# Optimization experiments

Hardware: AMD Instinct MI355X
Metric: run time of the kernel (lower is better)

Reference implementation:

```python
import jax, jax.numpy as jnp
import numpy as np

B, T, D = 32, 4096, 512  # batch, encoder timesteps t_k, attn_sz (== encoder dim == state_sz)


def setup_inputs() -> dict:
    key = jax.random.key(0)
    ks = jax.random.split(key, 7)
    scale = 1.0 / np.sqrt(D)
    return {
        "h_i": jax.random.normal(ks[0], (B, T, D), dtype=jnp.float32),
        "s_t": jax.random.normal(ks[1], (B, D), dtype=jnp.float32),
        "coverage": jax.random.uniform(ks[2], (B, T), dtype=jnp.float32),
        "W_h": jax.random.normal(ks[3], (D, D), dtype=jnp.float32) * scale,
        "W_s": jax.random.normal(ks[4], (D, D), dtype=jnp.float32) * scale,
        "b_s": jnp.zeros((D,), dtype=jnp.float32),
        "W_c": jax.random.normal(ks[5], (1, D), dtype=jnp.float32) * scale,
        "V": jax.random.normal(ks[6], (D, 1), dtype=jnp.float32) * scale,
    }


def reference(h_i, s_t, coverage, W_h, W_s, b_s, W_c, V):
    # enc_features: (B, T, D)
    enc_features = jnp.einsum("btd,de->bte", h_i, W_h)
    # dec_features: (B, D) broadcast over T
    dec_features = s_t @ W_s + b_s
    # coverage term: Dense(D) applied to coverage[..., None] -> outer product with W_c row
    cov_features = coverage[..., None] * W_c[0]  # (B, T, D)
    features = enc_features + dec_features[:, None, :] + cov_features
    # e_t = V(tanh(features)) squeezed to (B, T)
    e_t = jnp.einsum("bte,e->bt", jnp.tanh(features), V[:, 0])
    a_t = jax.nn.softmax(e_t, axis=1)  # (B, T)
    new_coverage = coverage + a_t
    # context = a_t^T h_i : (B, D)
    context_vector = jnp.einsum("bt,btd->bd", a_t, h_i)
    return context_vector, a_t, new_coverage
```

## Files before the change

kernel.cpp:

```cpp
#include <hip/hip_runtime.h>
#include <stdint.h>

#define B_ 32
#define T_ 4096
#define D_ 512
#define BT_ (B_*T_)

typedef __attribute__((ext_vector_type(8))) short bf16x8;
typedef __attribute__((ext_vector_type(4))) float f32x4;

__device__ __forceinline__ unsigned short f2bf(float f) {
    unsigned int u = __float_as_uint(f);
    u += 0x7FFFu + ((u >> 16) & 1u);
    return (unsigned short)(u >> 16);
}

__device__ __forceinline__ float tanh_fast(float x) {
    float e2 = __expf(2.0f * x);
    return 1.0f - 2.0f / (e2 + 1.0f);
}

__global__ __launch_bounds__(256) void k_conv_wh(const float* __restrict__ W_h,
                                                 unsigned short* __restrict__ wsb) {
    int tid = blockIdx.x * 256 + threadIdx.x;
    int l  = tid & 63;
    int kt = (tid >> 6) & 15;
    int nt = tid >> 10;
    int n  = nt * 16 + (l & 15);
    int k0 = kt * 32 + (l >> 4) * 8;
    unsigned int w[4];
#pragma unroll
    for (int q = 0; q < 4; ++q) {
        unsigned short lo = f2bf(W_h[(size_t)(k0 + 2*q)     * D_ + n]);
        unsigned short hi = f2bf(W_h[(size_t)(k0 + 2*q + 1) * D_ + n]);
        w[q] = (unsigned int)lo | ((unsigned int)hi << 16);
    }
    uint4 pk = {w[0], w[1], w[2], w[3]};
    ((uint4*)wsb)[tid] = pk;
}

__global__ __launch_bounds__(256) void k_dec(const float* __restrict__ s_t,
                                             const float* __restrict__ W_s,
                                             const float* __restrict__ b_s,
                                             float* __restrict__ dec) {
    int b = blockIdx.x;
    int c = threadIdx.x;
    float a0 = b_s[c], a1 = b_s[c + 256];
    const float* srow = s_t + b * D_;
    for (int k = 0; k < D_; ++k) {
        float s = srow[k];
        const float* wr = W_s + (size_t)k * D_;
        a0 = fmaf(s, wr[c], a0);
        a1 = fmaf(s, wr[c + 256], a1);
    }
    dec[b * D_ + c] = a0;
    dec[b * D_ + c + 256] = a1;
}

__global__ __launch_bounds__(512, 4) void k_main(const float* __restrict__ h_i,
                                                 const float* __restrict__ coverage,
                                                 const unsigned short* __restrict__ wsb,
                                                 const float* __restrict__ dec,
                                                 const float* __restrict__ W_c,
                                                 const float* __restrict__ V,
                                                 float* __restrict__ e_out) {
    __shared__ __align__(16) unsigned char As[65536];
    __shared__ float red[8][64];
    const int tid = threadIdx.x;
    const int w = tid >> 6, l = tid & 63;
    const int row0 = blockIdx.x * 64;
    const int b    = row0 >> 12;
    const int t0   = row0 & (T_ - 1);

#pragma unroll
    for (int i = 0; i < 8; ++i) {
        int row = i * 8 + w;
        const float* src = h_i + (size_t)(row0 + row) * D_ + l * 8;
        float4 f0 = *(const float4*)(src);
        float4 f1 = *(const float4*)(src + 4);
        uint4 pk;
        pk.x = (unsigned)f2bf(f0.x) | ((unsigned)f2bf(f0.y) << 16);
        pk.y = (unsigned)f2bf(f0.z) | ((unsigned)f2bf(f0.w) << 16);
        pk.z = (unsigned)f2bf(f1.x) | ((unsigned)f2bf(f1.y) << 16);
        pk.w = (unsigned)f2bf(f1.z) | ((unsigned)f2bf(f1.w) << 16);
        int kt   = l >> 2;
        int lam  = (row & 15) + 16 * (l & 3);
        int slot = (lam & 0x38) | ((lam & 7) ^ ((l & 3) << 1) ^ (kt & 1));
        int byte = (((row >> 4) * 16 + kt) << 10) + (slot << 4);
        *(uint4*)(As + byte) = pk;
    }
    __syncthreads();

    const int slotR = (l & 0x38) | ((l & 7) ^ (((l >> 4) & 3) << 1));

    f32x4 acc[4][4];
#pragma unroll
    for (int af = 0; af < 4; ++af)
#pragma unroll
        for (int j = 0; j < 4; ++j) acc[af][j] = (f32x4){0, 0, 0, 0};

    const uint4* bw = (const uint4*)wsb + ((w * 4) << 10) + l;

#pragma unroll 4
    for (int kt = 0; kt < 16; ++kt) {
        bf16x8 bv[4];
#pragma unroll
        for (int j = 0; j < 4; ++j) {
            uint4 braw = bw[(j << 10) + (kt << 6)];
            bv[j] = __builtin_bit_cast(bf16x8, braw);
        }
        int sl = (slotR ^ (kt & 1)) << 4;
#pragma unroll
        for (int af = 0; af < 4; ++af) {
            int byte = ((af * 16 + kt) << 10) + sl;
            uint4 araw = *(const uint4*)(As + byte);
            bf16x8 a = __builtin_bit_cast(bf16x8, araw);
#pragma unroll
            for (int j = 0; j < 4; ++j)
                acc[af][j] = __builtin_amdgcn_mfma_f32_16x16x32_bf16(a, bv[j], acc[af][j], 0, 0, 0);
        }
    }

    const int rgrp = (l >> 4) * 4;
    float cov_r[4][4];
#pragma unroll
    for (int af = 0; af < 4; ++af)
#pragma unroll
        for (int r = 0; r < 4; ++r)
            cov_r[af][r] = coverage[b * T_ + t0 + af * 16 + rgrp + r];

    float p[4][4] = {{0,0,0,0},{0,0,0,0},{0,0,0,0},{0,0,0,0}};
#pragma unroll
    for (int j = 0; j < 4; ++j) {
        int col = w * 64 + j * 16 + (l & 15);
        float dv = dec[b * D_ + col];
        float wc = W_c[col];
        float vv = V[col];
#pragma unroll
        for (int af = 0; af < 4; ++af)
#pragma unroll
            for (int r = 0; r < 4; ++r) {
                float x = acc[af][j][r] + dv + cov_r[af][r] * wc;
                p[af][r] += tanh_fast(x) * vv;
            }
    }

#pragma unroll
    for (int m = 1; m <= 8; m <<= 1)
#pragma unroll
        for (int af = 0; af < 4; ++af)
#pragma unroll
            for (int r = 0; r < 4; ++r)
                p[af][r] += __shfl_xor(p[af][r], m, 64);
    if ((l & 15) == 0) {
#pragma unroll
        for (int af = 0; af < 4; ++af)
#pragma unroll
            for (int r = 0; r < 4; ++r)
                red[w][af * 16 + rgrp + r] = p[af][r];
    }
    __syncthreads();
    if (tid < 64) {
        float e = red[0][tid] + red[1][tid] + red[2][tid] + red[3][tid]
                + red[4][tid] + red[5][tid] + red[6][tid] + red[7][tid];
        e_out[b * T_ + t0 + tid] = e;
    }
}

__global__ __launch_bounds__(256) void k_soft(const float* __restrict__ e_in,
                                              const float* __restrict__ coverage,
                                              float* __restrict__ out_at,
                                              float* __restrict__ out_cov) {
    int b = blockIdx.x, tid = threadIdx.x;
    __shared__ float red[4];
    float v[16];
    float m = -1e30f;
#pragma unroll
    for (int i = 0; i < 16; ++i) {
        v[i] = e_in[b * T_ + tid + i * 256];
        m = fmaxf(m, v[i]);
    }
#pragma unroll
    for (int mk = 1; mk <= 32; mk <<= 1) m = fmaxf(m, __shfl_xor(m, mk, 64));
    if ((tid & 63) == 0) red[tid >> 6] = m;
    __syncthreads();
    m = fmaxf(fmaxf(red[0], red[1]), fmaxf(red[2], red[3]));
    float s = 0.f;
#pragma unroll
    for (int i = 0; i < 16; ++i) { v[i] = expf(v[i] - m); s += v[i]; }
#pragma unroll
    for (int mk = 1; mk <= 32; mk <<= 1) s += __shfl_xor(s, mk, 64);
    __syncthreads();
    if ((tid & 63) == 0) red[tid >> 6] = s;
    __syncthreads();
    s = red[0] + red[1] + red[2] + red[3];
    float inv = 1.0f / s;
#pragma unroll
    for (int i = 0; i < 16; ++i) {
        int idx = b * T_ + tid + i * 256;
        float a = v[i] * inv;
        out_at[idx]  = a;
        out_cov[idx] = coverage[idx] + a;
    }
}

__global__ __launch_bounds__(256) void k_ctx(const float* __restrict__ h_i,
                                             const float* __restrict__ a_t,
                                             float* __restrict__ part) {
    int blk = blockIdx.x;
    int b = blk >> 6, s = blk & 63;
    int d0 = threadIdx.x * 2;
    const size_t base = ((size_t)b * T_ + (size_t)s * 64) * D_;
    const float* at = a_t + b * T_ + s * 64;
    float2 acc = {0.f, 0.f};
    for (int t = 0; t < 64; ++t) {
        float a = at[t];
        float2 h2 = *(const float2*)(h_i + base + (size_t)t * D_ + d0);
        acc.x = fmaf(a, h2.x, acc.x);
        acc.y = fmaf(a, h2.y, acc.y);
    }
    float* pp = part + (size_t)blk * D_ + d0;
    pp[0] = acc.x;
    pp[1] = acc.y;
}

__global__ __launch_bounds__(256) void k_comb(const float* __restrict__ part,
                                              float* __restrict__ out_ctx) {
    int idx = blockIdx.x * 256 + threadIdx.x;
    int b = idx >> 9, d = idx & 511;
    const float* pp = part + (size_t)b * 64 * D_ + d;
    float s = 0.f;
#pragma unroll 8
    for (int j = 0; j < 64; ++j) s += pp[(size_t)j * D_];
    out_ctx[idx] = s;
}

extern "C" void kernel_launch(void* const* d_in, const int* in_sizes, int n_in,
                              void* d_out, int out_size, void* d_ws, size_t ws_size,
                              hipStream_t stream) {
    const float* h_i      = (const float*)d_in[0];
    const float* s_t      = (const float*)d_in[1];
    const float* coverage = (const float*)d_in[2];
    const float* W_h      = (const float*)d_in[3];
    const float* W_s      = (const float*)d_in[4];
    const float* b_s      = (const float*)d_in[5];
    const float* W_c      = (const float*)d_in[6];
    const float* V        = (const float*)d_in[7];

    float* out_ctx = (float*)d_out;
    float* out_at  = out_ctx + B_ * D_;
    float* out_cov = out_at + BT_;

    unsigned short* wsb = (unsigned short*)d_ws;
    float* dec  = (float*)((char*)d_ws + 524288);
    float* part = dec + B_ * D_;

    k_conv_wh<<<128, 256, 0, stream>>>(W_h, wsb);
    k_dec<<<B_, 256, 0, stream>>>(s_t, W_s, b_s, dec);
    k_main<<<BT_ / 64, 512, 0, stream>>>(h_i, coverage, wsb, dec, W_c, V, out_at);
    k_soft<<<B_, 256, 0, stream>>>(out_at, coverage, out_at, out_cov);
    k_ctx<<<B_ * 64, 256, 0, stream>>>(h_i, out_at, part);
    k_comb<<<B_ * D_ / 256, 256, 0, stream>>>(part, out_ctx);
}
```

Measured before the change: 196.1 us.

## Split A-tile staging into two K halves and overlap second load with MFMA

```diff
diff --git a/kernel.cpp b/kernel.cpp
--- a/kernel.cpp
+++ b/kernel.cpp
@@ -72,54 +72,88 @@
     const int b    = row0 >> 12;
     const int t0   = row0 & (T_ - 1);
 
+    const int s_ktl  = l >> 3;
+    const int s_m    = ((l >> 1) & 3);
+    const int s_bits = (s_m << 4) | (w ^ (s_m << 1) ^ (l >> 3 & 1));
+    const int s_off  = (s_ktl << 10) + ((l & 1) << 3);
+
+    const int slotR = (l & 0x38) | ((l & 7) ^ (((l >> 4) & 3) << 1));
+
+    const uint4* bw = (const uint4*)wsb + ((w * 4) << 10) + l;
+
+    f32x4 acc[4][4];
+#pragma unroll
+    for (int af = 0; af < 4; ++af)
+#pragma unroll
+        for (int j = 0; j < 4; ++j) acc[af][j] = (f32x4){0, 0, 0, 0};
+
+    float4 L[8];
+#pragma unroll
+    for (int i = 0; i < 8; ++i)
+        L[i] = *(const float4*)(h_i + (size_t)(row0 + i * 8 + w) * D_ + l * 4);
+
+    unsigned char* A0 = As;
+    unsigned char* A1 = As + 32768;
 #pragma unroll
     for (int i = 0; i < 8; ++i) {
-        int row = i * 8 + w;
-        const float* src = h_i + (size_t)(row0 + row) * D_ + l * 8;
-        float4 f0 = *(const float4*)(src);
-        float4 f1 = *(const float4*)(src + 4);
-        uint4 pk;
-        pk.x = (unsigned)f2bf(f0.x) | ((unsigned)f2bf(f0.y) << 16);
-        pk.y = (unsigned)f2bf(f0.z) | ((unsigned)f2bf(f0.w) << 16);
-        pk.z = (unsigned)f2bf(f1.x) | ((unsigned)f2bf(f1.y) << 16);
-        pk.w = (unsigned)f2bf(f1.z) | ((unsigned)f2bf(f1.w) << 16);
-        int kt   = l >> 2;
-        int lam  = (row & 15) + 16 * (l & 3);
-        int slot = (lam & 0x38) | ((lam & 7) ^ ((l & 3) << 1) ^ (kt & 1));
-        int byte = (((row >> 4) * 16 + kt) << 10) + (slot << 4);
-        *(uint4*)(As + byte) = pk;
-    }
-    __syncthreads();
-
-    const int slotR = (l & 0x38) | ((l & 7) ^ (((l >> 4) & 3) << 1));
-
-    f32x4 acc[4][4];
-#pragma unroll
-    for (int af = 0; af < 4; ++af)
-#pragma unroll
-        for (int j = 0; j < 4; ++j) acc[af][j] = (f32x4){0, 0, 0, 0};
-
-    const uint4* bw = (const uint4*)wsb + ((w * 4) << 10) + l;
-
-#pragma unroll 4
-    for (int kt = 0; kt < 16; ++kt) {
-        bf16x8 bv[4];
-#pragma unroll
-        for (int j = 0; j < 4; ++j) {
-            uint4 braw = bw[(j << 10) + (kt << 6)];
-            bv[j] = __builtin_bit_cast(bf16x8, braw);
+        uint2 pk;
+        pk.x = (unsigned)f2bf(L[i].x) | ((unsigned)f2bf(L[i].y) << 16);
+        pk.y = (unsigned)f2bf(L[i].z) | ((unsigned)f2bf(L[i].w) << 16);
+        int slot = ((i & 1) << 3) | s_bits;
+        int byte = (((i >> 1) << 13)) + (slot << 4) + s_off;
+        *(uint2*)(A0 + byte) = pk;
+    }
+
+    float4 M[8];
+#pragma unroll
+    for (int i = 0; i < 8; ++i)
+        M[i] = *(const float4*)(h_i + (size_t)(row0 + i * 8 + w) * D_ + 256 + l * 4);
+
+    asm volatile("s_waitcnt lgkmcnt(0)" ::: "memory");
+    __builtin_amdgcn_s_barrier();
+
+    auto compute = [&](const unsigned char* Ab, int h8) {
+        uint4 bp[2][4];
+#pragma unroll
+        for (int j = 0; j < 4; ++j) bp[0][j] = bw[(j << 10) + ((h8 + 0) << 6)];
+#pragma unroll
+        for (int j = 0; j < 4; ++j) bp[1][j] = bw[(j << 10) + ((h8 + 1) << 6)];
+#pragma unroll
+        for (int ktl = 0; ktl < 8; ++ktl) {
+            const int sl = ((slotR ^ (ktl & 1)) << 4);
+#pragma unroll
+            for (int af = 0; af < 4; ++af) {
+                uint4 araw = *(const uint4*)(Ab + ((af * 8 + ktl) << 10) + sl);
+                bf16x8 a = __builtin_bit_cast(bf16x8, araw);
+#pragma unroll
+                for (int j = 0; j < 4; ++j) {
+                    bf16x8 bv = __builtin_bit_cast(bf16x8, bp[ktl & 1][j]);
+                    acc[af][j] = __builtin_amdgcn_mfma_f32_16x16x32_bf16(a, bv, acc[af][j], 0, 0, 0);
+                }
+            }
+            if (ktl < 6) {
+#pragma unroll
+                for (int j = 0; j < 4; ++j)
+                    bp[ktl & 1][j] = bw[(j << 10) + ((h8 + ktl + 2) << 6)];
+            }
         }
-        int sl = (slotR ^ (kt & 1)) << 4;
-#pragma unroll
-        for (int af = 0; af < 4; ++af) {
-            int byte = ((af * 16 + kt) << 10) + sl;
-            uint4 araw = *(const uint4*)(As + byte);
-            bf16x8 a = __builtin_bit_cast(bf16x8, araw);
-#pragma unroll
-            for (int j = 0; j < 4; ++j)
-                acc[af][j] = __builtin_amdgcn_mfma_f32_16x16x32_bf16(a, bv[j], acc[af][j], 0, 0, 0);
-        }
-    }
+    };
+
+    compute(A0, 0);
+
+#pragma unroll
+    for (int i = 0; i < 8; ++i) {
+        uint2 pk;
+        pk.x = (unsigned)f2bf(M[i].x) | ((unsigned)f2bf(M[i].y) << 16);
+        pk.y = (unsigned)f2bf(M[i].z) | ((unsigned)f2bf(M[i].w) << 16);
+        int slot = ((i & 1) << 3) | s_bits;
+        int byte = (((i >> 1) << 13)) + (slot << 4) + s_off;
+        *(uint2*)(A1 + byte) = pk;
+    }
+    asm volatile("s_waitcnt lgkmcnt(0)" ::: "memory");
+    __builtin_amdgcn_s_barrier();
+
+    compute(A1, 8);
 
     const int rgrp = (l >> 4) * 4;
     float cov_r[4][4];
```

After: 241.7 us. +23.3%, slower.

## Fuse context accumulation into attention-score kernel using unnormalized exp weights

Applied to the files above, without the earlier changes.

```diff
diff --git a/kernel.cpp b/kernel.cpp
--- a/kernel.cpp
+++ b/kernel.cpp
@@ -63,31 +63,41 @@
                                                  const float* __restrict__ dec,
                                                  const float* __restrict__ W_c,
                                                  const float* __restrict__ V,
-                                                 float* __restrict__ e_out) {
+                                                 float* __restrict__ e_out,
+                                                 float* __restrict__ part) {
     __shared__ __align__(16) unsigned char As[65536];
     __shared__ float red[8][64];
+    __shared__ float wexp[64];
     const int tid = threadIdx.x;
     const int w = tid >> 6, l = tid & 63;
     const int row0 = blockIdx.x * 64;
     const int b    = row0 >> 12;
     const int t0   = row0 & (T_ - 1);
 
+    float4 L0[8], L1[8];
 #pragma unroll
     for (int i = 0; i < 8; ++i) {
-        int row = i * 8 + w;
-        const float* src = h_i + (size_t)(row0 + row) * D_ + l * 8;
-        float4 f0 = *(const float4*)(src);
-        float4 f1 = *(const float4*)(src + 4);
-        uint4 pk;
-        pk.x = (unsigned)f2bf(f0.x) | ((unsigned)f2bf(f0.y) << 16);
-        pk.y = (unsigned)f2bf(f0.z) | ((unsigned)f2bf(f0.w) << 16);
-        pk.z = (unsigned)f2bf(f1.x) | ((unsigned)f2bf(f1.y) << 16);
-        pk.w = (unsigned)f2bf(f1.z) | ((unsigned)f2bf(f1.w) << 16);
-        int kt   = l >> 2;
-        int lam  = (row & 15) + 16 * (l & 3);
-        int slot = (lam & 0x38) | ((lam & 7) ^ ((l & 3) << 1) ^ (kt & 1));
-        int byte = (((row >> 4) * 16 + kt) << 10) + (slot << 4);
-        *(uint4*)(As + byte) = pk;
+        const float* src = h_i + (size_t)(row0 + i * 8 + w) * D_ + l * 8;
+        L0[i] = *(const float4*)(src);
+        L1[i] = *(const float4*)(src + 4);
+    }
+    {
+        const int kt   = l >> 2;
+        const int lam  = 16 * (l & 3);
+        const int sl_m = (l & 3) << 1;
+#pragma unroll
+        for (int i = 0; i < 8; ++i) {
+            int row = i * 8 + w;
+            uint4 pk;
+            pk.x = (unsigned)f2bf(L0[i].x) | ((unsigned)f2bf(L0[i].y) << 16);
+            pk.y = (unsigned)f2bf(L0[i].z) | ((unsigned)f2bf(L0[i].w) << 16);
+            pk.z = (unsigned)f2bf(L1[i].x) | ((unsigned)f2bf(L1[i].y) << 16);
+            pk.w = (unsigned)f2bf(L1[i].z) | ((unsigned)f2bf(L1[i].w) << 16);
+            int lamf = lam + (row & 15);
+            int slot = (lamf & 0x38) | ((lamf & 7) ^ sl_m ^ (kt & 1));
+            int byte = (((row >> 4) * 16 + kt) << 10) + (slot << 4);
+            *(uint4*)(As + byte) = pk;
+        }
     }
     __syncthreads();
 
@@ -101,23 +111,30 @@
 
     const uint4* bw = (const uint4*)wsb + ((w * 4) << 10) + l;
 
-#pragma unroll 4
-    for (int kt = 0; kt < 16; ++kt) {
-        bf16x8 bv[4];
-#pragma unroll
-        for (int j = 0; j < 4; ++j) {
-            uint4 braw = bw[(j << 10) + (kt << 6)];
-            bv[j] = __builtin_bit_cast(bf16x8, braw);
-        }
-        int sl = (slotR ^ (kt & 1)) << 4;
-#pragma unroll
-        for (int af = 0; af < 4; ++af) {
-            int byte = ((af * 16 + kt) << 10) + sl;
-            uint4 araw = *(const uint4*)(As + byte);
-            bf16x8 a = __builtin_bit_cast(bf16x8, araw);
-#pragma unroll
-            for (int j = 0; j < 4; ++j)
-                acc[af][j] = __builtin_amdgcn_mfma_f32_16x16x32_bf16(a, bv[j], acc[af][j], 0, 0, 0);
+    {
+        uint4 bp[2][4];
+#pragma unroll
+        for (int j = 0; j < 4; ++j) bp[0][j] = bw[(j << 10)];
+#pragma unroll
+        for (int j = 0; j < 4; ++j) bp[1][j] = bw[(j << 10) + (1 << 6)];
+#pragma unroll
+        for (int kt = 0; kt < 16; ++kt) {
+            const int sl = ((slotR ^ (kt & 1)) << 4);
+#pragma unroll
+            for (int af = 0; af < 4; ++af) {
+                uint4 araw = *(const uint4*)(As + ((af * 16 + kt) << 10) + sl);
+                bf16x8 a = __builtin_bit_cast(bf16x8, araw);
+#pragma unroll
+                for (int j = 0; j < 4; ++j) {
+                    bf16x8 bv = __builtin_bit_cast(bf16x8, bp[kt & 1][j]);
+                    acc[af][j] = __builtin_amdgcn_mfma_f32_16x16x32_bf16(a, bv, acc[af][j], 0, 0, 0);
+                }
+            }
+            if (kt < 14) {
+#pragma unroll
+                for (int j = 0; j < 4; ++j)
+                    bp[kt & 1][j] = bw[(j << 10) + ((kt + 2) << 6)];
+            }
         }
     }
 
@@ -164,13 +181,33 @@
         float e = red[0][tid] + red[1][tid] + red[2][tid] + red[3][tid]
                 + red[4][tid] + red[5][tid] + red[6][tid] + red[7][tid];
         e_out[b * T_ + t0 + tid] = e;
+        wexp[tid] = __expf(e);
+    }
+    __syncthreads();
+
+    {
+        const int d    = tid;
+        const int ktg  = d >> 5;
+        const int mq   = (d >> 3) & 3;
+        const int base2 = ((mq << 4) | (((mq << 1) ^ (ktg & 1)) & 7)) << 4;
+        const unsigned char* Ag = As + (ktg << 10) + ((d & 7) << 1);
+        float cacc = 0.f;
+#pragma unroll
+        for (int t = 0; t < 64; ++t) {
+            int byte = ((t >> 4) << 14) + (base2 ^ ((t & 15) << 4));
+            unsigned short u = *(const unsigned short*)(Ag + byte);
+            float hv = __uint_as_float(((unsigned)u) << 16);
+            cacc = fmaf(wexp[t], hv, cacc);
+        }
+        part[(size_t)blockIdx.x * D_ + d] = cacc;
     }
 }
 
 __global__ __launch_bounds__(256) void k_soft(const float* __restrict__ e_in,
                                               const float* __restrict__ coverage,
                                               float* __restrict__ out_at,
-                                              float* __restrict__ out_cov) {
+                                              float* __restrict__ out_cov,
+                                              float* __restrict__ Sb) {
     int b = blockIdx.x, tid = threadIdx.x;
     __shared__ float red[4];
     float v[16];
@@ -194,6 +231,7 @@
     if ((tid & 63) == 0) red[tid >> 6] = s;
     __syncthreads();
     s = red[0] + red[1] + red[2] + red[3];
+    if (tid == 0) Sb[b] = __expf(m) * s;
     float inv = 1.0f / s;
 #pragma unroll
     for (int i = 0; i < 16; ++i) {
@@ -204,27 +242,8 @@
     }
 }
 
-__global__ __launch_bounds__(256) void k_ctx(const float* __restrict__ h_i,
-                                             const float* __restrict__ a_t,
-                                             float* __restrict__ part) {
-    int blk = blockIdx.x;
-    int b = blk >> 6, s = blk & 63;
-    int d0 = threadIdx.x * 2;
-    const size_t base = ((size_t)b * T_ + (size_t)s * 64) * D_;
-    const float* at = a_t + b * T_ + s * 64;
-    float2 acc = {0.f, 0.f};
-    for (int t = 0; t < 64; ++t) {
-        float a = at[t];
-        float2 h2 = *(const float2*)(h_i + base + (size_t)t * D_ + d0);
-        acc.x = fmaf(a, h2.x, acc.x);
-        acc.y = fmaf(a, h2.y, acc.y);
-    }
-    float* pp = part + (size_t)blk * D_ + d0;
-    pp[0] = acc.x;
-    pp[1] = acc.y;
-}
-
 __global__ __launch_bounds__(256) void k_comb(const float* __restrict__ part,
+                                              const float* __restrict__ Sb,
                                               float* __restrict__ out_ctx) {
     int idx = blockIdx.x * 256 + threadIdx.x;
     int b = idx >> 9, d = idx & 511;
@@ -232,7 +251,7 @@
     float s = 0.f;
 #pragma unroll 8
     for (int j = 0; j < 64; ++j) s += pp[(size_t)j * D_];
-    out_ctx[idx] = s;
+    out_ctx[idx] = s / Sb[b];
 }
 
 extern "C" void kernel_launch(void* const* d_in, const int* in_sizes, int n_in,
@@ -254,11 +273,11 @@
     unsigned short* wsb = (unsigned short*)d_ws;
     float* dec  = (float*)((char*)d_ws + 524288);
     float* part = dec + B_ * D_;
+    float* Sb   = part + (size_t)BT_ / 64 * D_;
 
     k_conv_wh<<<128, 256, 0, stream>>>(W_h, wsb);
     k_dec<<<B_, 256, 0, stream>>>(s_t, W_s, b_s, dec);
-    k_main<<<BT_ / 64, 512, 0, stream>>>(h_i, coverage, wsb, dec, W_c, V, out_at);
-    k_soft<<<B_, 256, 0, stream>>>(out_at, coverage, out_at, out_cov);
-    k_ctx<<<B_ * 64, 256, 0, stream>>>(h_i, out_at, part);
-    k_comb<<<B_ * D_ / 256, 256, 0, stream>>>(part, out_ctx);
-}
+    k_main<<<BT_ / 64, 512, 0, stream>>>(h_i, coverage, wsb, dec, W_c, V, out_at, part);
+    k_soft<<<B_, 256, 0, stream>>>(out_at, coverage, out_at, out_cov, Sb);
+    k_comb<<<B_ * D_ / 256, 256, 0, stream>>>(part, Sb, out_ctx);
+}
```

Measured after the change: 168.4 us. -14.1%, faster.
